# Kernel optimization log

Hardware: AMD Instinct MI355X
Metric: run time of the kernel (lower is better)

Reference implementation:

```python
import jax, jax.numpy as jnp
import numpy as np

N_NODES = 100_000
N_EDGES = 1_600_000
HIDDEN = 32


def setup_inputs() -> dict:
    key = jax.random.key(0)
    ks = jax.random.split(key, 8)
    pos = jax.random.normal(ks[0], (N_NODES, 3), dtype=jnp.float32)
    edge_index = jax.random.randint(ks[1], (2, N_EDGES), 0, N_NODES, dtype=jnp.int64)
    batch = jnp.zeros((N_NODES,), dtype=jnp.int64)
    # layer 1 MLP: Linear(3+3 -> 32) -> ReLU -> Linear(32 -> 32)
    W1 = jax.random.normal(ks[2], (6, HIDDEN), dtype=jnp.float32) * (1.0 / np.sqrt(6))
    b1 = jnp.zeros((HIDDEN,), dtype=jnp.float32)
    W2 = jax.random.normal(ks[3], (HIDDEN, HIDDEN), dtype=jnp.float32) * (1.0 / np.sqrt(HIDDEN))
    b2 = jnp.zeros((HIDDEN,), dtype=jnp.float32)
    # layer 2 MLP: Linear(32+3 -> 32) -> ReLU -> Linear(32 -> 32)
    W3 = jax.random.normal(ks[4], (HIDDEN + 3, HIDDEN), dtype=jnp.float32) * (1.0 / np.sqrt(HIDDEN + 3))
    b3 = jnp.zeros((HIDDEN,), dtype=jnp.float32)
    W4 = jax.random.normal(ks[5], (HIDDEN, HIDDEN), dtype=jnp.float32) * (1.0 / np.sqrt(HIDDEN))
    b4 = jnp.zeros((HIDDEN,), dtype=jnp.float32)
    return {"pos": pos, "edge_index": edge_index, "batch": batch,
            "W1": W1, "b1": b1, "W2": W2, "b2": b2,
            "W3": W3, "b3": b3, "W4": W4, "b4": b4}


def _pointnet_layer(h, rel, src, dst, n_nodes, Wa, ba, Wb, bb):
    # per-edge: concat(h_j, pos_j - pos_i) -> Linear -> ReLU -> Linear, then max-scatter into i
    e = jnp.concatenate([h[src], rel], axis=-1)             # [E, in+3]
    m = jax.nn.relu(e @ Wa + ba) @ Wb + bb                  # [E, out]
    agg = jax.ops.segment_max(m, dst, num_segments=n_nodes)  # [N, out], -inf for isolated nodes
    return jnp.where(jnp.isfinite(agg), agg, 0.0)


def reference(pos, edge_index, batch, W1, b1, W2, b2, W3, b3, W4, b4):
    src = edge_index[0]  # j (source)
    dst = edge_index[1]  # i (target, aggregation index)
    n_nodes = pos.shape[0]
    rel = pos[src] - pos[dst]  # [E, 3]
    h = jax.nn.relu(_pointnet_layer(pos, rel, src, dst, n_nodes, W1, b1, W2, b2))
    h = jax.nn.relu(_pointnet_layer(h, rel, src, dst, n_nodes, W3, b3, W4, b4))
    return h
```

## Files before the change

kernel.cpp:

```cpp
#include <hip/hip_runtime.h>
#include <hip/hip_bf16.h>
#include <stdint.h>


#define BS 256
#define EBS 512
#define K1_EDGES 4096
#define RB 64

typedef float v2f __attribute__((ext_vector_type(2)));
typedef __attribute__((ext_vector_type(8))) short bf16x8;
typedef __attribute__((ext_vector_type(16))) float f32x16;
typedef __bf16 bf16v2 __attribute__((ext_vector_type(2)));

__device__ __forceinline__ unsigned ordenc(float f) {
    unsigned u = __float_as_uint(f);
    return (u & 0x80000000u) ? ~u : (u | 0x80000000u);
}
__device__ __forceinline__ float orddec(unsigned o) {
    unsigned u = (o & 0x80000000u) ? (o ^ 0x80000000u) : ~o;
    return __uint_as_float(u);
}
#define ORD_NEG_INF 0x007FFFFFu
#define SRC_MASK 0xFFFFFu

__device__ __forceinline__ unsigned cvt2(float x, float y) {
    v2f v = {x, y};
    bf16v2 b = __builtin_convertvector(v, bf16v2);
    return __builtin_bit_cast(unsigned, b);
}
__device__ __forceinline__ float bflo(unsigned u) { return __uint_as_float(u << 16); }
__device__ __forceinline__ float bfhi(unsigned u) { return __uint_as_float(u & 0xFFFF0000u); }

__device__ __forceinline__ uint4 mk_frag(uint4 ua, float4 v0, float4 v1) {
    uint4 o;
    o.x = cvt2(fmaxf(bflo(ua.x) - v0.x, 0.0f), fmaxf(bfhi(ua.x) - v0.y, 0.0f));
    o.y = cvt2(fmaxf(bflo(ua.y) - v0.z, 0.0f), fmaxf(bfhi(ua.y) - v0.w, 0.0f));
    o.z = cvt2(fmaxf(bflo(ua.z) - v1.x, 0.0f), fmaxf(bfhi(ua.z) - v1.y, 0.0f));
    o.w = cvt2(fmaxf(bflo(ua.w) - v1.z, 0.0f), fmaxf(bfhi(ua.w) - v1.w, 0.0f));
    return o;
}

__global__ __launch_bounds__(BS) void setup_kernel(
    const int* __restrict__ ei, int E, int NRP, int* __restrict__ blockHist,
    const float* __restrict__ pos, const float* __restrict__ Wa, const float* __restrict__ ba,
    unsigned* __restrict__ Ubf, float* __restrict__ V, int N, int NB1, int NBn,
    const float* __restrict__ Wb2, const float* __restrict__ Wb4,
    unsigned* __restrict__ WbtG) {
    __shared__ int hist[2048];
    const int tid = threadIdx.x;
    const int b = blockIdx.x;
    if (b < NB1) {
        for (int r = tid; r < 2048; r += BS) hist[r] = 0;
        __syncthreads();
        const int base = b * K1_EDGES;
        const int M = min(K1_EDGES, E - base);
        for (int i = tid; i < M; i += BS) atomicAdd(&hist[ei[E + base + i] >> 6], 1);
        __syncthreads();
        for (int r = tid; r < NRP; r += BS) blockHist[b * NRP + r] = hist[r];
    } else if (b < NB1 + NBn) {
        const int n = (b - NB1) * BS + tid;
        if (n >= N) return;
        const float p[3] = {pos[3 * n], pos[3 * n + 1], pos[3 * n + 2]};
        v2f u[16], v[16];
#pragma unroll
        for (int g = 0; g < 16; ++g) {
            u[g] = *reinterpret_cast<const v2f*>(&ba[g * 2]);
            v2f z = {0.0f, 0.0f};
            v[g] = z;
        }
#pragma unroll
        for (int i = 0; i < 3; ++i) {
            const v2f f = {p[i], p[i]};
#pragma unroll
            for (int g = 0; g < 16; ++g) {
                const v2f wA = *reinterpret_cast<const v2f*>(&Wa[i * 32 + g * 2]);
                const v2f wB = *reinterpret_cast<const v2f*>(&Wa[(i + 3) * 32 + g * 2]);
                u[g] = __builtin_elementwise_fma(f, wA + wB, u[g]);
                v[g] = __builtin_elementwise_fma(f, wB, v[g]);
            }
        }
        uint4* Up = reinterpret_cast<uint4*>(Ubf + (size_t)n * 16);
        float4* Vp = reinterpret_cast<float4*>(V + (size_t)n * 32);
#pragma unroll
        for (int q = 0; q < 4; ++q) {
            uint4 o;
            o.x = cvt2(u[4 * q + 0].x, u[4 * q + 0].y);
            o.y = cvt2(u[4 * q + 1].x, u[4 * q + 1].y);
            o.z = cvt2(u[4 * q + 2].x, u[4 * q + 2].y);
            o.w = cvt2(u[4 * q + 3].x, u[4 * q + 3].y);
            Up[q] = o;
        }
#pragma unroll
        for (int q = 0; q < 8; ++q)
            Vp[q] = make_float4(v[2 * q].x, v[2 * q].y, v[2 * q + 1].x, v[2 * q + 1].y);
    } else {
        if (tid < 128) {
            const int layer = tid >> 6;
            const int t = tid & 63;
            const int lnp = t & 31;
            const int hp = t >> 5;
            const float* Wb = layer ? Wb4 : Wb2;
            unsigned* dst = WbtG + layer * 512 + t * 8;
#pragma unroll
            for (int q = 0; q < 4; ++q) {
                const int p = 4 * hp + q;
                dst[q] = cvt2(Wb[(2 * p) * 32 + lnp], Wb[(2 * p + 1) * 32 + lnp]);
                dst[4 + q] = cvt2(Wb[(2 * p + 16) * 32 + lnp], Wb[(2 * p + 17) * 32 + lnp]);
            }
        }
    }
}

__global__ __launch_bounds__(512) void off_scan_kernel(const int* __restrict__ blockHist,
                                                       int NB1, int NRP,
                                                       int* __restrict__ off,
                                                       int* __restrict__ total) {
    const int r = (blockIdx.x * 512 + threadIdx.x) >> 6;
    const int lane = threadIdx.x & 63;
    if (r >= NRP) return;
    int carry = 0;
    const int chunks = (NB1 + 63) / 64;
    for (int c = 0; c < chunks; ++c) {
        const int b = c * 64 + lane;
        const int v = (b < NB1) ? blockHist[b * NRP + r] : 0;
        int x = v;
#pragma unroll
        for (int d = 1; d < 64; d <<= 1) {
            int y = __shfl_up(x, d, 64);
            if (lane >= d) x += y;
        }
        if (b < NB1) off[b * NRP + r] = carry + (x - v);
        carry += __shfl(x, 63, 64);
    }
    if (lane == 0) total[r] = carry;
}

__global__ __launch_bounds__(1024) void range_scan_kernel(const int* __restrict__ total,
                                                          int NRP, int* __restrict__ rangeBase) {
    __shared__ int s[2048];
    const int t = threadIdx.x;
    const int v0 = (t < NRP) ? total[t] : 0;
    const int v1 = (t + 1024 < NRP) ? total[t + 1024] : 0;
    s[t] = v0;
    s[t + 1024] = v1;
    __syncthreads();
    for (int off = 1; off < 2048; off <<= 1) {
        const int a0 = (t >= off) ? s[t - off] : 0;
        const int a1 = (t + 1024 >= off) ? s[t + 1024 - off] : 0;
        __syncthreads();
        s[t] += a0;
        s[t + 1024] += a1;
        __syncthreads();
    }
    if (t < NRP) rangeBase[t] = s[t] - v0;
    if (t + 1024 < NRP) rangeBase[t + 1024] = s[t + 1024] - v1;
}

__global__ __launch_bounds__(BS) void bucket_scatter_kernel(
    const int* __restrict__ ei, int E, int NRP, const int* __restrict__ off,
    const int* __restrict__ rangeBase, unsigned* __restrict__ sedgeB) {
    __shared__ unsigned stage[K1_EDGES];
    __shared__ unsigned short rng[K1_EDGES];
    __shared__ unsigned short inv[K1_EDGES];
    __shared__ int hist[2048], start[2048], cursor[2048];
    __shared__ int ts[BS];
    const int tid = threadIdx.x;
    for (int r = tid; r < 2048; r += BS) hist[r] = 0;
    __syncthreads();
    const int base = blockIdx.x * K1_EDGES;
    const int M = min(K1_EDGES, E - base);
    for (int i = tid; i < M; i += BS) {
        const int src = ei[base + i];
        const int dst = ei[E + base + i];
        const int r = dst >> 6;
        stage[i] = (unsigned)src | ((unsigned)(dst & 63) << 20);
        rng[i] = (unsigned short)r;
        atomicAdd(&hist[r], 1);
    }
    __syncthreads();
    {
        const int i0 = tid * 8;
        int lv[8];
        int tsum = 0;
#pragma unroll
        for (int k = 0; k < 8; ++k) {
            lv[k] = hist[i0 + k];
            tsum += lv[k];
        }
        ts[tid] = tsum;
        __syncthreads();
        for (int off2 = 1; off2 < BS; off2 <<= 1) {
            int add = (tid >= off2) ? ts[tid - off2] : 0;
            __syncthreads();
            ts[tid] += add;
            __syncthreads();
        }
        int run = ts[tid] - tsum;
#pragma unroll
        for (int k = 0; k < 8; ++k) {
            start[i0 + k] = run;
            cursor[i0 + k] = run;
            run += lv[k];
        }
    }
    __syncthreads();
    for (int i = tid; i < M; i += BS) {
        const int pos = atomicAdd(&cursor[rng[i]], 1);
        inv[pos] = (unsigned short)i;
    }
    __syncthreads();
    const int* offb = off + blockIdx.x * NRP;
    for (int j = tid; j < M; j += BS) {
        const int i = inv[j];
        const int r = rng[i];
        sedgeB[rangeBase[r] + offb[r] + (j - start[r])] = stage[i];
    }
}

template <int MODE>
__global__ __launch_bounds__(EBS, 6) void edge_range_kernel(
    const unsigned* __restrict__ Ubf, const float4* __restrict__ V,
    const unsigned* __restrict__ sedgeB, const int* __restrict__ rangeBase,
    const int* __restrict__ total, const unsigned* __restrict__ WbtG,
    const float* __restrict__ bb, const float* __restrict__ pos,
    const float* __restrict__ Wa2, const float* __restrict__ ba2,
    unsigned* __restrict__ Ubf2, float* __restrict__ Vbuf2,
    float* __restrict__ out, int N) {
    __shared__ unsigned aggL[2048];
    __shared__ __align__(16) float4 vlds[576];
    __shared__ unsigned dstw[8][16];

    const int tid = threadIdx.x;
    const int r = blockIdx.x;
    const int base = rangeBase[r];
    const int M = total[r];
    const int last = M - 1;

    const int l = tid & 63;
    const int w = tid >> 6;
    const int half = l >> 5;
    const int ln = l & 31;

#pragma unroll
    for (int i = 0; i < 4; ++i) aggL[tid + i * EBS] = ORD_NEG_INF;

    {
        const float4* Vg = V + ((size_t)r << 9);
        const int vmax = min(512, (N - (r << 6)) * 8);
        if (tid < vmax) vlds[(tid >> 3) * 9 + (tid & 7)] = Vg[tid];
    }

    const uint4 bu0 = *reinterpret_cast<const uint4*>(WbtG + l * 8);
    const uint4 bu1 = *reinterpret_cast<const uint4*>(WbtG + l * 8 + 4);
    const float bbn = bb[ln];
    __syncthreads();

    const int nch = (M + EBS - 1) >> 9;
    unsigned pk = 0;
    if (64 * w < M) pk = sedgeB[base + min(64 * w + l, last)];
    for (int c = 0; c < nch; ++c) {
        unsigned npk = 0;
        const int ncb = (c + 1) << 9;
        const bool nextAct = (c + 1 < nch) && (ncb + 64 * w < M);
        if (nextAct) npk = sedgeB[base + min(ncb + 64 * w + l, last)];
        if ((c << 9) + 64 * w < M) {
            reinterpret_cast<unsigned char*>(dstw[w])[l] = (unsigned char)(pk >> 20);

            const unsigned pkA = __shfl(pk, ln, 64);
            const unsigned pkB = __shfl(pk, 32 + ln, 64);
            uint4 au00, au01, au10, au11;
            {
                const uint4* Up = reinterpret_cast<const uint4*>(Ubf + (size_t)(pkA & SRC_MASK) * 16);
                const float4* Vr = &vlds[(pkA >> 20) * 9];
                au00 = mk_frag(Up[half], Vr[2 * half], Vr[2 * half + 1]);
                au01 = mk_frag(Up[2 + half], Vr[4 + 2 * half], Vr[5 + 2 * half]);
            }
            {
                const uint4* Up = reinterpret_cast<const uint4*>(Ubf + (size_t)(pkB & SRC_MASK) * 16);
                const float4* Vr = &vlds[(pkB >> 20) * 9];
                au10 = mk_frag(Up[half], Vr[2 * half], Vr[2 * half + 1]);
                au11 = mk_frag(Up[2 + half], Vr[4 + 2 * half], Vr[5 + 2 * half]);
            }

            f32x16 c0, c1;
#pragma unroll
            for (int i = 0; i < 16; ++i) {
                c0[i] = bbn;
                c1[i] = bbn;
            }
            c0 = __builtin_amdgcn_mfma_f32_32x32x16_bf16(
                __builtin_bit_cast(bf16x8, au00), __builtin_bit_cast(bf16x8, bu0), c0, 0, 0, 0);
            c0 = __builtin_amdgcn_mfma_f32_32x32x16_bf16(
                __builtin_bit_cast(bf16x8, au01), __builtin_bit_cast(bf16x8, bu1), c0, 0, 0, 0);
            c1 = __builtin_amdgcn_mfma_f32_32x32x16_bf16(
                __builtin_bit_cast(bf16x8, au10), __builtin_bit_cast(bf16x8, bu0), c1, 0, 0, 0);
            c1 = __builtin_amdgcn_mfma_f32_32x32x16_bf16(
                __builtin_bit_cast(bf16x8, au11), __builtin_bit_cast(bf16x8, bu1), c1, 0, 0, 0);

            const unsigned* dw = dstw[w];
#pragma unroll
            for (int g = 0; g < 4; ++g) {
                const unsigned p0 = dw[2 * g + half];
                const unsigned p1 = dw[8 + 2 * g + half];
                {
                    const float v0 = c0[4 * g + 0], v1 = c0[4 * g + 1];
                    const float v2 = c0[4 * g + 2], v3 = c0[4 * g + 3];
                    if (p0 == (p0 & 0xFFu) * 0x01010101u) {
                        const float m = fmaxf(fmaxf(v0, v1), fmaxf(v2, v3));
                        atomicMax(&aggL[((p0 & 0x3Fu) << 5) | ln], ordenc(m));
                    } else {
                        atomicMax(&aggL[(((p0 >> 0) & 0x3Fu) << 5) | ln], ordenc(v0));
                        atomicMax(&aggL[(((p0 >> 8) & 0x3Fu) << 5) | ln], ordenc(v1));
                        atomicMax(&aggL[(((p0 >> 16) & 0x3Fu) << 5) | ln], ordenc(v2));
                        atomicMax(&aggL[(((p0 >> 24) & 0x3Fu) << 5) | ln], ordenc(v3));
                    }
                }
                {
                    const float v0 = c1[4 * g + 0], v1 = c1[4 * g + 1];
                    const float v2 = c1[4 * g + 2], v3 = c1[4 * g + 3];
                    if (p1 == (p1 & 0xFFu) * 0x01010101u) {
                        const float m = fmaxf(fmaxf(v0, v1), fmaxf(v2, v3));
                        atomicMax(&aggL[((p1 & 0x3Fu) << 5) | ln], ordenc(m));
                    } else {
                        atomicMax(&aggL[(((p1 >> 0) & 0x3Fu) << 5) | ln], ordenc(v0));
                        atomicMax(&aggL[(((p1 >> 8) & 0x3Fu) << 5) | ln], ordenc(v1));
                        atomicMax(&aggL[(((p1 >> 16) & 0x3Fu) << 5) | ln], ordenc(v2));
                        atomicMax(&aggL[(((p1 >> 24) & 0x3Fu) << 5) | ln], ordenc(v3));
                    }
                }
            }
        }
        pk = npk;
    }
    __syncthreads();

    if (MODE == 0) {
        const int idx = tid * 4;
        const int node = (r << 6) + (idx >> 5);
        if (node < N) {
            float4 o;
            o.x = fmaxf(orddec(aggL[idx + 0]), 0.0f);
            o.y = fmaxf(orddec(aggL[idx + 1]), 0.0f);
            o.z = fmaxf(orddec(aggL[idx + 2]), 0.0f);
            o.w = fmaxf(orddec(aggL[idx + 3]), 0.0f);
            *reinterpret_cast<float4*>(out + (size_t)node * 32 + (idx & 31)) = o;
        }
    } else {
        const int node_l = tid >> 3;
        const int qq = tid & 7;
        const int node = (r << 6) + node_l;
        if (node < N) {
            const unsigned* row = &aggL[node_l << 5];
            float h[32];
#pragma unroll
            for (int i = 0; i < 32; ++i) h[i] = fmaxf(orddec(row[i]), 0.0f);
            const float pp[3] = {pos[3 * node], pos[3 * node + 1], pos[3 * node + 2]};
            v2f u[2], v[2];
#pragma unroll
            for (int g = 0; g < 2; ++g) {
                u[g] = *reinterpret_cast<const v2f*>(&ba2[4 * qq + 2 * g]);
                v2f z = {0.0f, 0.0f};
                v[g] = z;
            }
#pragma unroll
            for (int i = 0; i < 32; ++i) {
                const v2f f = {h[i], h[i]};
#pragma unroll
                for (int g = 0; g < 2; ++g) {
                    const v2f wv =
                        *reinterpret_cast<const v2f*>(&Wa2[i * 32 + 4 * qq + 2 * g]);
                    u[g] = __builtin_elementwise_fma(f, wv, u[g]);
                }
            }
#pragma unroll
            for (int i = 0; i < 3; ++i) {
                const v2f f = {pp[i], pp[i]};
#pragma unroll
                for (int g = 0; g < 2; ++g) {
                    const v2f wv =
                        *reinterpret_cast<const v2f*>(&Wa2[(32 + i) * 32 + 4 * qq + 2 * g]);
                    u[g] = __builtin_elementwise_fma(f, wv, u[g]);
                    v[g] = __builtin_elementwise_fma(f, wv, v[g]);
                }
            }
            uint2 o;
            o.x = cvt2(u[0].x, u[0].y);
            o.y = cvt2(u[1].x, u[1].y);
            *reinterpret_cast<uint2*>(Ubf2 + (size_t)node * 16 + 2 * qq) = o;
            *reinterpret_cast<float4*>(Vbuf2 + (size_t)node * 32 + 4 * qq) =
                make_float4(v[0].x, v[0].y, v[1].x, v[1].y);
        }
    }
}

extern "C" void kernel_launch(void* const* d_in, const int* in_sizes, int n_in,
                              void* d_out, int out_size, void* d_ws, size_t ws_size,
                              hipStream_t stream) {
    const float* pos = (const float*)d_in[0];
    const int* ei = (const int*)d_in[1];
    const float* W1 = (const float*)d_in[3];
    const float* b1 = (const float*)d_in[4];
    const float* W2 = (const float*)d_in[5];
    const float* b2 = (const float*)d_in[6];
    const float* W3 = (const float*)d_in[7];
    const float* b3 = (const float*)d_in[8];
    const float* W4 = (const float*)d_in[9];
    const float* b4 = (const float*)d_in[10];

    const int E = in_sizes[1] / 2;
    const int N = in_sizes[0] / 3;
    const int n32 = N * 32;
    const int NPAD = ((N + BS - 1) / BS) * BS;
    const int NR = (N + RB - 1) / RB;
    const int NRP = ((NR + 15) / 16) * 16;
    const int NB1 = (E + K1_EDGES - 1) / K1_EDGES;
    const int BH = NB1 * NRP;

    int* blockHist = (int*)d_ws;
    int* off = blockHist + BH;
    int* total = off + BH;
    int* rangeBase = total + NRP;
    unsigned* sedgeB = (unsigned*)(rangeBase + NRP);
    unsigned* Ubf = (unsigned*)(sedgeB + E);
    float* Vbuf = (float*)(Ubf + (size_t)NPAD * 16);
    unsigned* Ubf2 = (unsigned*)(Vbuf + n32);
    float* Vbuf2 = (float*)(Ubf2 + (size_t)NPAD * 16);
    unsigned* WbtG = (unsigned*)(Vbuf2 + n32);

    const int NBn = (N + BS - 1) / BS;

    setup_kernel<<<NB1 + NBn + 1, BS, 0, stream>>>(ei, E, NRP, blockHist, pos, W1, b1, Ubf,
                                                   Vbuf, N, NB1, NBn, W2, W4, WbtG);
    off_scan_kernel<<<(NRP * 64 + 511) / 512, 512, 0, stream>>>(blockHist, NB1, NRP, off,
                                                                total);
    range_scan_kernel<<<1, 1024, 0, stream>>>(total, NRP, rangeBase);
    bucket_scatter_kernel<<<NB1, BS, 0, stream>>>(ei, E, NRP, off, rangeBase, sedgeB);

    edge_range_kernel<1><<<NR, EBS, 0, stream>>>(Ubf, (const float4*)Vbuf, sedgeB, rangeBase,
                                                 total, WbtG, b2, pos, W3, b3, Ubf2, Vbuf2,
                                                 nullptr, N);
    edge_range_kernel<0><<<NR, EBS, 0, stream>>>(Ubf2, (const float4*)Vbuf2, sedgeB,
                                                 rangeBase, total, WbtG + 512, b4, nullptr,
                                                 nullptr, nullptr, nullptr, nullptr,
                                                 (float*)d_out, N);
}
```

Measured before the change: 201.0 us.

## Fold range scan into off-scan via last-block flag; use non-negative max encoding

After: 239.5 us. 1.19x slower.

```diff
diff --git a/kernel.cpp b/kernel.cpp
--- a/kernel.cpp
+++ b/kernel.cpp
@@ -13,15 +13,6 @@
 typedef __attribute__((ext_vector_type(16))) float f32x16;
 typedef __bf16 bf16v2 __attribute__((ext_vector_type(2)));
 
-__device__ __forceinline__ unsigned ordenc(float f) {
-    unsigned u = __float_as_uint(f);
-    return (u & 0x80000000u) ? ~u : (u | 0x80000000u);
-}
-__device__ __forceinline__ float orddec(unsigned o) {
-    unsigned u = (o & 0x80000000u) ? (o ^ 0x80000000u) : ~o;
-    return __uint_as_float(u);
-}
-#define ORD_NEG_INF 0x007FFFFFu
 #define SRC_MASK 0xFFFFFu
 
 __device__ __forceinline__ unsigned cvt2(float x, float y) {
@@ -33,11 +24,21 @@
 __device__ __forceinline__ float bfhi(unsigned u) { return __uint_as_float(u & 0xFFFF0000u); }
 
 __device__ __forceinline__ uint4 mk_frag(uint4 ua, float4 v0, float4 v1) {
+    const v2f z = {0.0f, 0.0f};
     uint4 o;
-    o.x = cvt2(fmaxf(bflo(ua.x) - v0.x, 0.0f), fmaxf(bfhi(ua.x) - v0.y, 0.0f));
-    o.y = cvt2(fmaxf(bflo(ua.y) - v0.z, 0.0f), fmaxf(bfhi(ua.y) - v0.w, 0.0f));
-    o.z = cvt2(fmaxf(bflo(ua.z) - v1.x, 0.0f), fmaxf(bfhi(ua.z) - v1.y, 0.0f));
-    o.w = cvt2(fmaxf(bflo(ua.w) - v1.z, 0.0f), fmaxf(bfhi(ua.w) - v1.w, 0.0f));
+    v2f a;
+    a = (v2f){bflo(ua.x), bfhi(ua.x)} - (v2f){v0.x, v0.y};
+    a = __builtin_elementwise_max(a, z);
+    o.x = cvt2(a.x, a.y);
+    a = (v2f){bflo(ua.y), bfhi(ua.y)} - (v2f){v0.z, v0.w};
+    a = __builtin_elementwise_max(a, z);
+    o.y = cvt2(a.x, a.y);
+    a = (v2f){bflo(ua.z), bfhi(ua.z)} - (v2f){v1.x, v1.y};
+    a = __builtin_elementwise_max(a, z);
+    o.z = cvt2(a.x, a.y);
+    a = (v2f){bflo(ua.w), bfhi(ua.w)} - (v2f){v1.z, v1.w};
+    a = __builtin_elementwise_max(a, z);
+    o.w = cvt2(a.x, a.y);
     return o;
 }
 
@@ -46,7 +47,7 @@
     const float* __restrict__ pos, const float* __restrict__ Wa, const float* __restrict__ ba,
     unsigned* __restrict__ Ubf, float* __restrict__ V, int N, int NB1, int NBn,
     const float* __restrict__ Wb2, const float* __restrict__ Wb4,
-    unsigned* __restrict__ WbtG) {
+    unsigned* __restrict__ WbtG, unsigned* __restrict__ done) {
     __shared__ int hist[2048];
     const int tid = threadIdx.x;
     const int b = blockIdx.x;
@@ -108,6 +109,8 @@
                 dst[q] = cvt2(Wb[(2 * p) * 32 + lnp], Wb[(2 * p + 1) * 32 + lnp]);
                 dst[4 + q] = cvt2(Wb[(2 * p + 16) * 32 + lnp], Wb[(2 * p + 17) * 32 + lnp]);
             }
+        } else if (tid == 128) {
+            *done = 0u;
         }
     }
 }
@@ -115,46 +118,59 @@
 __global__ __launch_bounds__(512) void off_scan_kernel(const int* __restrict__ blockHist,
                                                        int NB1, int NRP,
                                                        int* __restrict__ off,
-                                                       int* __restrict__ total) {
+                                                       int* __restrict__ total,
+                                                       int* __restrict__ rangeBase,
+                                                       unsigned* __restrict__ done) {
     const int r = (blockIdx.x * 512 + threadIdx.x) >> 6;
     const int lane = threadIdx.x & 63;
-    if (r >= NRP) return;
-    int carry = 0;
-    const int chunks = (NB1 + 63) / 64;
-    for (int c = 0; c < chunks; ++c) {
-        const int b = c * 64 + lane;
-        const int v = (b < NB1) ? blockHist[b * NRP + r] : 0;
-        int x = v;
-#pragma unroll
-        for (int d = 1; d < 64; d <<= 1) {
-            int y = __shfl_up(x, d, 64);
-            if (lane >= d) x += y;
-        }
-        if (b < NB1) off[b * NRP + r] = carry + (x - v);
-        carry += __shfl(x, 63, 64);
-    }
-    if (lane == 0) total[r] = carry;
-}
-
-__global__ __launch_bounds__(1024) void range_scan_kernel(const int* __restrict__ total,
-                                                          int NRP, int* __restrict__ rangeBase) {
-    __shared__ int s[2048];
+    if (r < NRP) {
+        int carry = 0;
+        const int chunks = (NB1 + 63) / 64;
+        for (int c = 0; c < chunks; ++c) {
+            const int b = c * 64 + lane;
+            const int v = (b < NB1) ? blockHist[b * NRP + r] : 0;
+            int x = v;
+#pragma unroll
+            for (int d = 1; d < 64; d <<= 1) {
+                int y = __shfl_up(x, d, 64);
+                if (lane >= d) x += y;
+            }
+            if (b < NB1) off[b * NRP + r] = carry + (x - v);
+            carry += __shfl(x, 63, 64);
+        }
+        if (lane == 0) total[r] = carry;
+    }
+    __shared__ unsigned lastFlag;
+    __shared__ int s4[512];
+    __threadfence();
+    __syncthreads();
+    if (threadIdx.x == 0) lastFlag = (atomicAdd(done, 1u) + 1u == gridDim.x) ? 1u : 0u;
+    __syncthreads();
+    if (!lastFlag) return;
     const int t = threadIdx.x;
-    const int v0 = (t < NRP) ? total[t] : 0;
-    const int v1 = (t + 1024 < NRP) ? total[t + 1024] : 0;
-    s[t] = v0;
-    s[t + 1024] = v1;
-    __syncthreads();
-    for (int off = 1; off < 2048; off <<= 1) {
-        const int a0 = (t >= off) ? s[t - off] : 0;
-        const int a1 = (t + 1024 >= off) ? s[t + 1024 - off] : 0;
+    int v4[4];
+    int sum = 0;
+#pragma unroll
+    for (int k = 0; k < 4; ++k) {
+        const int idx = t * 4 + k;
+        v4[k] = (idx < NRP) ? total[idx] : 0;
+        sum += v4[k];
+    }
+    s4[t] = sum;
+    __syncthreads();
+    for (int o2 = 1; o2 < 512; o2 <<= 1) {
+        int add = (t >= o2) ? s4[t - o2] : 0;
         __syncthreads();
-        s[t] += a0;
-        s[t + 1024] += a1;
+        s4[t] += add;
         __syncthreads();
     }
-    if (t < NRP) rangeBase[t] = s[t] - v0;
-    if (t + 1024 < NRP) rangeBase[t + 1024] = s[t + 1024] - v1;
+    int run = s4[t] - sum;
+#pragma unroll
+    for (int k = 0; k < 4; ++k) {
+        const int idx = t * 4 + k;
+        if (idx < NRP) rangeBase[idx] = run;
+        run += v4[k];
+    }
 }
 
 __global__ __launch_bounds__(BS) void bucket_scatter_kernel(
@@ -243,7 +259,7 @@
     const int ln = l & 31;
 
 #pragma unroll
-    for (int i = 0; i < 4; ++i) aggL[tid + i * EBS] = ORD_NEG_INF;
+    for (int i = 0; i < 4; ++i) aggL[tid + i * EBS] = 0u;
 
     {
         const float4* Vg = V + ((size_t)r << 9);
@@ -308,12 +324,17 @@
                     const float v2 = c0[4 * g + 2], v3 = c0[4 * g + 3];
                     if (p0 == (p0 & 0xFFu) * 0x01010101u) {
                         const float m = fmaxf(fmaxf(v0, v1), fmaxf(v2, v3));
-                        atomicMax(&aggL[((p0 & 0x3Fu) << 5) | ln], ordenc(m));
+                        atomicMax(&aggL[((p0 & 0x3Fu) << 5) | ln],
+                                  __float_as_uint(fmaxf(m, 0.0f)));
                     } else {
-                        atomicMax(&aggL[(((p0 >> 0) & 0x3Fu) << 5) | ln], ordenc(v0));
-                        atomicMax(&aggL[(((p0 >> 8) & 0x3Fu) << 5) | ln], ordenc(v1));
-                        atomicMax(&aggL[(((p0 >> 16) & 0x3Fu) << 5) | ln], ordenc(v2));
-                        atomicMax(&aggL[(((p0 >> 24) & 0x3Fu) << 5) | ln], ordenc(v3));
+                        atomicMax(&aggL[(((p0 >> 0) & 0x3Fu) << 5) | ln],
+                                  __float_as_uint(fmaxf(v0, 0.0f)));
+                        atomicMax(&aggL[(((p0 >> 8) & 0x3Fu) << 5) | ln],
+                                  __float_as_uint(fmaxf(v1, 0.0f)));
+                        atomicMax(&aggL[(((p0 >> 16) & 0x3Fu) << 5) | ln],
+                                  __float_as_uint(fmaxf(v2, 0.0f)));
+                        atomicMax(&aggL[(((p0 >> 24) & 0x3Fu) << 5) | ln],
+                                  __float_as_uint(fmaxf(v3, 0.0f)));
                     }
                 }
                 {
@@ -321,12 +342,17 @@
                     const float v2 = c1[4 * g + 2], v3 = c1[4 * g + 3];
                     if (p1 == (p1 & 0xFFu) * 0x01010101u) {
                         const float m = fmaxf(fmaxf(v0, v1), fmaxf(v2, v3));
-                        atomicMax(&aggL[((p1 & 0x3Fu) << 5) | ln], ordenc(m));
+                        atomicMax(&aggL[((p1 & 0x3Fu) << 5) | ln],
+                                  __float_as_uint(fmaxf(m, 0.0f)));
                     } else {
-                        atomicMax(&aggL[(((p1 >> 0) & 0x3Fu) << 5) | ln], ordenc(v0));
-                        atomicMax(&aggL[(((p1 >> 8) & 0x3Fu) << 5) | ln], ordenc(v1));
-                        atomicMax(&aggL[(((p1 >> 16) & 0x3Fu) << 5) | ln], ordenc(v2));
-                        atomicMax(&aggL[(((p1 >> 24) & 0x3Fu) << 5) | ln], ordenc(v3));
+                        atomicMax(&aggL[(((p1 >> 0) & 0x3Fu) << 5) | ln],
+                                  __float_as_uint(fmaxf(v0, 0.0f)));
+                        atomicMax(&aggL[(((p1 >> 8) & 0x3Fu) << 5) | ln],
+                                  __float_as_uint(fmaxf(v1, 0.0f)));
+                        atomicMax(&aggL[(((p1 >> 16) & 0x3Fu) << 5) | ln],
+                                  __float_as_uint(fmaxf(v2, 0.0f)));
+                        atomicMax(&aggL[(((p1 >> 24) & 0x3Fu) << 5) | ln],
+                                  __float_as_uint(fmaxf(v3, 0.0f)));
                     }
                 }
             }
@@ -340,10 +366,10 @@
         const int node = (r << 6) + (idx >> 5);
         if (node < N) {
             float4 o;
-            o.x = fmaxf(orddec(aggL[idx + 0]), 0.0f);
-            o.y = fmaxf(orddec(aggL[idx + 1]), 0.0f);
-            o.z = fmaxf(orddec(aggL[idx + 2]), 0.0f);
-            o.w = fmaxf(orddec(aggL[idx + 3]), 0.0f);
+            o.x = __uint_as_float(aggL[idx + 0]);
+            o.y = __uint_as_float(aggL[idx + 1]);
+            o.z = __uint_as_float(aggL[idx + 2]);
+            o.w = __uint_as_float(aggL[idx + 3]);
             *reinterpret_cast<float4*>(out + (size_t)node * 32 + (idx & 31)) = o;
         }
     } else {
@@ -354,7 +380,7 @@
             const unsigned* row = &aggL[node_l << 5];
             float h[32];
 #pragma unroll
-            for (int i = 0; i < 32; ++i) h[i] = fmaxf(orddec(row[i]), 0.0f);
+            for (int i = 0; i < 32; ++i) h[i] = __uint_as_float(row[i]);
             const float pp[3] = {pos[3 * node], pos[3 * node + 1], pos[3 * node + 2]};
             v2f u[2], v[2];
 #pragma unroll
@@ -421,8 +447,9 @@
     int* off = blockHist + BH;
     int* total = off + BH;
     int* rangeBase = total + NRP;
-    unsigned* sedgeB = (unsigned*)(rangeBase + NRP);
-    unsigned* Ubf = (unsigned*)(sedgeB + E);
+    unsigned* done = (unsigned*)(rangeBase + NRP);
+    unsigned* sedgeB = done + 4;
+    unsigned* Ubf = sedgeB + E;
     float* Vbuf = (float*)(Ubf + (size_t)NPAD * 16);
     unsigned* Ubf2 = (unsigned*)(Vbuf + n32);
     float* Vbuf2 = (float*)(Ubf2 + (size_t)NPAD * 16);
@@ -431,10 +458,9 @@
     const int NBn = (N + BS - 1) / BS;
 
     setup_kernel<<<NB1 + NBn + 1, BS, 0, stream>>>(ei, E, NRP, blockHist, pos, W1, b1, Ubf,
-                                                   Vbuf, N, NB1, NBn, W2, W4, WbtG);
+                                                   Vbuf, N, NB1, NBn, W2, W4, WbtG, done);
     off_scan_kernel<<<(NRP * 64 + 511) / 512, 512, 0, stream>>>(blockHist, NB1, NRP, off,
-                                                                total);
-    range_scan_kernel<<<1, 1024, 0, stream>>>(total, NRP, rangeBase);
+                                                                total, rangeBase, done);
     bucket_scatter_kernel<<<NB1, BS, 0, stream>>>(ei, E, NRP, off, rangeBase, sedgeB);
 
     edge_range_kernel<1><<<NR, EBS, 0, stream>>>(Ubf, (const float4*)Vbuf, sedgeB, rangeBase,
```
